# Performance work log

Measured on AMD Instinct MI355X. Metric: run time of the kernel, lower is better.

## Reference

```python
import jax, jax.numpy as jnp
import numpy as np

NUM_BRANCH = 4
KERNEL_SIZES = (1, 3, 5, 7)
NUM_CLASSES = 1000
IN_C = 256
OUT_C = 256


def _cond_conv(x, w, emb, y):
    # x: [B,C,H,W], w: [O,I,k,k], emb: [num_classes,O], y: [B]
    out = jax.lax.conv_general_dilated(
        x, w, window_strides=(1, 1), padding='SAME',
        dimension_numbers=('NCHW', 'OIHW', 'NCHW'))
    return out + emb[y][:, :, None, None]


def setup_inputs() -> dict:
    key = jax.random.key(0)
    ks = jax.random.split(key, 2 + 2 * NUM_BRANCH)
    B, H = 64, 32
    inp = {
        'x': jax.random.normal(ks[0], (B, IN_C, H, H), dtype=jnp.float32),
        'y': jax.random.randint(ks[1], (B,), 0, NUM_CLASSES, dtype=jnp.int64),
        'sample_arc': jax.random.randint(jax.random.fold_in(key, 7), (B,), 0, NUM_BRANCH, dtype=jnp.int64),
    }
    for i, k in enumerate(KERNEL_SIZES):
        fan_in = IN_C * k * k
        inp[f'w{i}'] = jax.random.normal(ks[2 + 2 * i], (OUT_C, IN_C, k, k), dtype=jnp.float32) / np.sqrt(fan_in)
        inp[f'e{i}'] = jax.random.normal(ks[3 + 2 * i], (NUM_CLASSES, OUT_C), dtype=jnp.float32) * 0.02
    return inp


def reference(x, y, sample_arc, w0, w1, w2, w3, e0, e1, e2, e3):
    ws = (w0, w1, w2, w3)
    es = (e0, e1, e2, e3)
    # Compute every branch for every sample (as the original module does),
    # stack along branch dim: [B, num_branch, O, H, W]
    branch_out = jnp.stack([_cond_conv(x, w, e, y) for w, e in zip(ws, es)], axis=1)
    onehot = jax.nn.one_hot(sample_arc, NUM_BRANCH, dtype=x.dtype)  # [B, num_branch]
    # mask-and-sum (one-hot multiply then reduce over branch dim)
    return jnp.einsum('bn,bnchw->bchw', onehot, branch_out)
```

## Files before the change

### kernel.cpp

```cpp
#include <hip/hip_runtime.h>


typedef unsigned short ushort_t;
typedef __attribute__((ext_vector_type(8))) short short8;
typedef __attribute__((ext_vector_type(4))) float f32x4;

#define CIN   256
#define COUT  256
#define HH    32
#define WW    32
#define HW    1024

#define XT_ELEMS   16777216
#define WT_OFF_0   0
#define WT_OFF_1   65536
#define WT_OFF_2   655360
#define WT_OFF_3   2293760
#define WT_ELEMS   5505024
#define TILE_BYTE_OFF ((size_t)(XT_ELEMS + WT_ELEMS) * 2)
#define MAX_TILES  2048
#define WS_NEEDED  (TILE_BYTE_OFF + MAX_TILES * 2 + 64)

#define XS_R_STRIDE 1216
#define XS_C_STRIDE 32
#define XS_ELEMS    12160
#define WR_ELEMS    24576
#define TRASH_ELEMS 2048

__device__ inline ushort_t f2bf(float f) {
    unsigned x = __builtin_bit_cast(unsigned, f);
    unsigned r = (x + 0x7FFFu + ((x >> 16) & 1u)) >> 16;
    return (ushort_t)r;
}

__global__ __launch_bounds__(256) void prep_kernel(
    const float* __restrict__ x,
    const float* __restrict__ w0, const float* __restrict__ w1,
    const float* __restrict__ w2, const float* __restrict__ w3,
    const int* __restrict__ y, const int* __restrict__ arc,
    const float* __restrict__ e0, const float* __restrict__ e1,
    const float* __restrict__ e2, const float* __restrict__ e3,
    float* __restrict__ out,
    ushort_t* __restrict__ xt, ushort_t* __restrict__ wt,
    ushort_t* __restrict__ tiles, unsigned* __restrict__ cnt) {
    __shared__ float lds[2 * 32 * 49];
    const int blk = blockIdx.x;
    const int tid = threadIdx.x;

    if (blk < 4096) {
        const int a   = blk >> 10;
        const int cc  = (blk >> 7) & 7;
        const int oc0 = (blk & 127) * 2;
        const int kk  = (a == 0) ? 1 : (a == 1) ? 9 : (a == 2) ? 25 : 49;
        const float* __restrict__ w = (a == 0) ? w0 : (a == 1) ? w1
                                    : (a == 2) ? w2 : w3;
        const size_t woff = (a == 0) ? WT_OFF_0 : (a == 1) ? WT_OFF_1
                          : (a == 2) ? WT_OFF_2 : WT_OFF_3;
        const int ckk = 32 * kk;
#pragma unroll
        for (int ocq = 0; ocq < 2; ++ocq) {
            const float* src = w + ((size_t)((oc0 + ocq) * CIN + cc * 32)) * kk;
            for (int i = tid; i < ckk; i += 256) lds[ocq * ckk + i] = src[i];
        }
        __syncthreads();
        ushort_t* dst = wt + woff;
        const int F = 2 * kk * 32;
        for (int j = tid; j < F; j += 256) {
            const int ci  = j & 31;
            const int t2  = j >> 5;
            const int khw = t2 % kk;
            const int ocq = t2 / kk;
            dst[((size_t)(cc * kk + khw) * COUT + oc0 + ocq) * 32 + ci] =
                f2bf(lds[ocq * ckk + ci * kk + khw]);
        }
    } else if (blk < 6144) {
        const int id = (blk - 4096) * 256 + tid;
        const int hw = id & 1023;
        const int cc = (id >> 10) & 7;
        const int b  = id >> 13;
        const float* src = x + ((size_t)(b * CIN + cc * 32)) * HW + hw;
        ushort_t* dst = xt + ((size_t)((b * 8 + cc) * HW + hw)) * 32;
#pragma unroll
        for (int v = 0; v < 4; ++v) {
            short8 o;
#pragma unroll
            for (int j = 0; j < 8; ++j)
                o[j] = (short)f2bf(src[(size_t)(v * 8 + j) * HW]);
            *(short8*)(dst + v * 8) = o;
        }
    } else if (blk < 10240) {
        const int z   = blk - 6144;
        const int b   = z >> 6;
        const int a   = arc[b];
        if (a < 2) return;
        const int oc  = (z & 63) * 4 + (tid >> 6);
        const int i   = tid & 63;
        const int cls = y[b];
        const float* __restrict__ e = (a == 2) ? e2 : e3;
        const float ev = e[(size_t)cls * COUT + oc];
        float4 v = make_float4(ev, ev, ev, ev);
        float* ob = out + ((size_t)(b * COUT + oc)) * HW + i * 16;
#pragma unroll
        for (int k = 0; k < 4; ++k) *(float4*)(ob + k * 4) = v;
    } else if (tid < 64) {
        const int lane = tid;
        const int ab = (int)arc[lane];
        unsigned long long m[4];
#pragma unroll
        for (int v = 0; v < 4; ++v) m[v] = __ballot(ab == v);
        int gt = 0;
#pragma unroll
        for (int v = 1; v < 4; ++v) if (v > ab) gt += __popcll(m[v]);
        const unsigned long long eq = (ab == 0) ? m[0] : (ab == 1) ? m[1]
                                    : (ab == 2) ? m[2] : m[3];
        const unsigned long long lower = (lane == 0) ? 0ull
                                       : (~0ull >> (64 - lane));
        const int rank = gt + __popcll(eq & lower);
        const int nh   = __popcll(m[2]) + __popcll(m[3]);
        const bool heavy = (ab >= 2);
        const int myCnt = heavy ? 16 : 8;
        const int start = heavy ? 16 * rank : 16 * nh + 8 * (rank - nh);
        for (int j = 0; j < myCnt; ++j)
            tiles[start + j] = (ushort_t)((lane << 5) | j);
        if (lane == 0) { cnt[0] = 0u; cnt[1] = (unsigned)(512 + 8 * nh); }
    }
}

template <int K, int NCC, bool ATOMIC>
__device__ void conv_body(const ushort_t* __restrict__ xt,
                          const ushort_t* __restrict__ wtb,
                          const float* __restrict__ eb,
                          int b, int cls, int cc0, int r0,
                          float* __restrict__ out,
                          ushort_t* xs, ushort_t* wr, ushort_t* trash) {
    constexpr int KK   = K * K;
    constexpr int PAD  = K / 2;
    constexpr int R    = 4 + 2 * PAD;
    constexpr int ITER = (R * 128) / 256;

    const int tid  = threadIdx.x;
    const int wave = tid >> 6;
    const int lane = tid & 63;
    const int ln   = lane & 15;
    const int q    = lane >> 4;

    f32x4 acc[4][8];
#pragma unroll
    for (int mt = 0; mt < 4; ++mt)
#pragma unroll
        for (int nt = 0; nt < 8; ++nt) acc[mt][nt] = (f32x4)0.0f;

    ushort_t* wrw = wr + wave * (3 * 2048);
    const ushort_t* wsrc = wtb + (size_t)wave * 2048 + (size_t)lane * 8;

    const int t0   = cc0 * KK;
    const int TEND = (cc0 + NCC) * KK;

    auto issue = [&](int idx, ushort_t* dst) {
#pragma unroll
        for (int mt = 0; mt < 4; ++mt)
            __builtin_amdgcn_global_load_lds(
                (const __attribute__((address_space(1))) void*)
                    (wsrc + (size_t)idx * 8192 + mt * 512),
                (__attribute__((address_space(3))) void*)
                    (dst + mt * 512),
                16, 0, 0);
    };

    issue(t0, wrw); issue(t0 + 1, wrw + 2048); issue(t0 + 2, wrw + 4096);

    const ushort_t* xsrc = xt + ((size_t)b * 8) * (HW * 32);

    int rs = 0;
    for (int cc2 = 0; cc2 < NCC; ++cc2) {
        const int cc = cc0 + cc2;
        __syncthreads();
#pragma unroll
        for (int i = 0; i < ITER; ++i) {
            const int id = tid + i * 256;
            const int r  = id >> 7;
            const int gw = (id >> 2) & 31;
            const int g4 = id & 3;
            const int gr = r0 - PAD + r;
            short8 v = (short8)0;
            if (gr >= 0 && gr < HH)
                v = *(const short8*)&xsrc[((size_t)(cc * HW + gr * WW + gw)) * 32 + g4 * 8];
            *(short8*)&xs[r * XS_R_STRIDE + (gw + 3) * XS_C_STRIDE + g4 * 8] = v;
        }
        __syncthreads();

#pragma unroll 1
        for (int kh = 0; kh < K; ++kh) {
#pragma unroll
            for (int kw = 0; kw < K; ++kw) {
                const int t = cc * KK + kh * K + kw;
                asm volatile("s_waitcnt vmcnt(8)" ::: "memory");
                __builtin_amdgcn_sched_barrier(0);
                short8 afc[4];
#pragma unroll
                for (int mt = 0; mt < 4; ++mt)
                    afc[mt] = *(const short8*)&wrw[rs * 2048 + mt * 512 + ln * 32 + q * 8];
                asm volatile("s_waitcnt lgkmcnt(0)" ::: "memory");
                __builtin_amdgcn_sched_barrier(0);
                const bool real = (t + 3 < TEND);
                issue(real ? (t + 3) : t0, real ? (wrw + rs * 2048) : trash);
                short8 bf[8];
#pragma unroll
                for (int nt = 0; nt < 8; ++nt) {
                    const int rl = (nt >> 1) + kh;
                    const int c  = (nt & 1) * 16 + ln + 3 + (kw - PAD);
                    bf[nt] = *(const short8*)&xs[rl * XS_R_STRIDE + c * XS_C_STRIDE + q * 8];
                }
#pragma unroll
                for (int mt = 0; mt < 4; ++mt)
#pragma unroll
                    for (int nt = 0; nt < 8; ++nt)
                        acc[mt][nt] = __builtin_amdgcn_mfma_f32_16x16x32_bf16(
                            afc[mt], bf[nt], acc[mt][nt], 0, 0, 0);
                rs = (rs == 2) ? 0 : rs + 1;
            }
        }
    }

#pragma unroll
    for (int mt = 0; mt < 4; ++mt) {
#pragma unroll
        for (int i = 0; i < 4; ++i) {
            const int oc = wave * 64 + mt * 16 + q * 4 + i;
            float* ob = out + ((size_t)(b * COUT + oc)) * HW;
            if (ATOMIC) {
#pragma unroll
                for (int nt = 0; nt < 8; ++nt) {
                    const int row = r0 + (nt >> 1);
                    const int col = (nt & 1) * 16 + ln;
                    atomicAdd(&ob[row * WW + col], acc[mt][nt][i]);
                }
            } else {
                const float ev = eb[(size_t)cls * COUT + oc];
#pragma unroll
                for (int nt = 0; nt < 8; ++nt) {
                    const int row = r0 + (nt >> 1);
                    const int col = (nt & 1) * 16 + ln;
                    ob[row * WW + col] = acc[mt][nt][i] + ev;
                }
            }
        }
    }
}

__global__ __launch_bounds__(256, 2) void conv_mfma(
    const ushort_t* __restrict__ xt, const ushort_t* __restrict__ wt,
    const int* __restrict__ y, const int* __restrict__ arc,
    const float* __restrict__ e0, const float* __restrict__ e1,
    const float* __restrict__ e2, const float* __restrict__ e3,
    float* __restrict__ out,
    const ushort_t* __restrict__ tiles, unsigned* __restrict__ cnt) {
    __shared__ ushort_t xs[XS_ELEMS];
    __shared__ ushort_t wr[WR_ELEMS];
    __shared__ ushort_t trash[TRASH_ELEMS];
    __shared__ int t_sh;
    const int tid = threadIdx.x;
    const unsigned T = cnt[1];

    for (int i = tid; i < 240; i += 256) {
        const int g    = i & 3;
        const int cell = i >> 2;
        const int cidx = cell % 6;
        const int r    = cell / 6;
        const int col  = (cidx < 3) ? cidx : cidx + 32;
        *(short8*)&xs[r * XS_R_STRIDE + col * XS_C_STRIDE + g * 8] = (short8)0;
    }

    for (;;) {
        if (tid == 0) {
            const unsigned t = atomicAdd(cnt, 1u);
            t_sh = (t < T) ? (int)tiles[t] : -1;
        }
        __syncthreads();
        const int e = t_sh;
        __syncthreads();
        if (e < 0) break;

        const int b   = e >> 5;
        const int j   = e & 31;
        const int a   = __builtin_amdgcn_readfirstlane(arc[b]);
        const int cls = __builtin_amdgcn_readfirstlane(y[b]);
        switch (a) {
            case 0:  conv_body<1, 8, false>(xt, wt + WT_OFF_0, e0, b, cls,
                                            0, (j & 7) << 2, out, xs, wr, trash); break;
            case 1:  conv_body<3, 8, false>(xt, wt + WT_OFF_1, e1, b, cls,
                                            0, (j & 7) << 2, out, xs, wr, trash); break;
            case 2:  conv_body<5, 4, true>(xt, wt + WT_OFF_2, e2, b, cls,
                                           (j & 1) << 2, (j >> 1) << 2, out, xs, wr, trash); break;
            default: conv_body<7, 4, true>(xt, wt + WT_OFF_3, e3, b, cls,
                                           (j & 1) << 2, (j >> 1) << 2, out, xs, wr, trash); break;
        }
    }
}

__global__ __launch_bounds__(256) void cond_conv_direct(
    const float* __restrict__ x, const int* __restrict__ y,
    const int* __restrict__ arc,
    const float* __restrict__ w0, const float* __restrict__ e0,
    const float* __restrict__ w1, const float* __restrict__ e1,
    const float* __restrict__ w2, const float* __restrict__ e2,
    const float* __restrict__ w3, const float* __restrict__ e3,
    float* __restrict__ out) {
    const int b   = blockIdx.x >> 4;
    const int o0  = (blockIdx.x & 15) << 4;
    const int tid = threadIdx.x;
    const int col  = tid & 31;
    const int row0 = tid >> 5;
    int a   = __builtin_amdgcn_readfirstlane(arc[b]);
    int cls = __builtin_amdgcn_readfirstlane(y[b]);
    const int k   = (a == 0) ? 1 : (a == 1) ? 3 : (a == 2) ? 5 : 7;
    const int kk  = k * k;
    const int pad = k >> 1;
    const float* __restrict__ wp = (a == 0) ? w0 : (a == 1) ? w1 : (a == 2) ? w2 : w3;
    const float* __restrict__ ep = (a == 0) ? e0 : (a == 1) ? e1 : (a == 2) ? e2 : e3;
    __shared__ float xsh[8 * HW];
    float acc[16][4];
#pragma unroll
    for (int o = 0; o < 16; ++o)
#pragma unroll
        for (int p = 0; p < 4; ++p) acc[o][p] = 0.f;
    const float* xb = x + (size_t)b * CIN * HW;
    for (int c0 = 0; c0 < CIN; c0 += 8) {
        __syncthreads();
        const float4* src = (const float4*)(xb + c0 * HW);
        float4* dst = (float4*)xsh;
#pragma unroll
        for (int i = 0; i < 8; ++i) dst[tid + (i << 8)] = src[tid + (i << 8)];
        __syncthreads();
        for (int kh = 0; kh < k; ++kh) {
            const int dh = kh - pad;
            int raddr[4]; bool rok[4];
#pragma unroll
            for (int p = 0; p < 4; ++p) {
                const int rr = row0 + 8 * p + dh;
                rok[p] = (rr >= 0) && (rr < HH);
                raddr[p] = (rok[p] ? rr : 0) * WW;
            }
            for (int kw = 0; kw < k; ++kw) {
                const int cc2 = col + kw - pad;
                const bool cok = (cc2 >= 0) && (cc2 < WW);
                const int cofs = cok ? cc2 : 0;
                const int khw = kh * k + kw;
#pragma unroll
                for (int ci = 0; ci < 8; ++ci) {
                    float xv[4];
#pragma unroll
                    for (int p = 0; p < 4; ++p) {
                        const float v = xsh[ci * HW + raddr[p] + cofs];
                        xv[p] = (rok[p] && cok) ? v : 0.f;
                    }
                    const float* wb = wp + (size_t)o0 * CIN * kk + (size_t)(c0 + ci) * kk + khw;
#pragma unroll
                    for (int o = 0; o < 16; ++o) {
                        const float wsv = wb[(size_t)o * CIN * kk];
#pragma unroll
                        for (int p = 0; p < 4; ++p) acc[o][p] += wsv * xv[p];
                    }
                }
            }
        }
    }
    const float* erow = ep + (size_t)cls * COUT + o0;
    float* ob = out + (size_t)(b * COUT + o0) * HW;
#pragma unroll
    for (int o = 0; o < 16; ++o) {
        const float ev = erow[o];
#pragma unroll
        for (int p = 0; p < 4; ++p)
            ob[o * HW + (row0 + 8 * p) * WW + col] = acc[o][p] + ev;
    }
}

extern "C" void kernel_launch(void* const* d_in, const int* in_sizes, int n_in,
                              void* d_out, int out_size, void* d_ws, size_t ws_size,
                              hipStream_t stream) {
    const float* x   = (const float*)d_in[0];
    const int*   y   = (const int*)  d_in[1];
    const int*   arc = (const int*)  d_in[2];
    const float* w0  = (const float*)d_in[3];
    const float* e0  = (const float*)d_in[4];
    const float* w1  = (const float*)d_in[5];
    const float* e1  = (const float*)d_in[6];
    const float* w2  = (const float*)d_in[7];
    const float* e2  = (const float*)d_in[8];
    const float* w3  = (const float*)d_in[9];
    const float* e3  = (const float*)d_in[10];
    float* out = (float*)d_out;
    const int B = in_sizes[1];

    if (ws_size >= WS_NEEDED && B == 64) {
        ushort_t* xt    = (ushort_t*)d_ws;
        ushort_t* wt    = xt + XT_ELEMS;
        ushort_t* tiles = (ushort_t*)((char*)d_ws + TILE_BYTE_OFF);
        unsigned* cnt   = (unsigned*)((char*)d_ws + TILE_BYTE_OFF + MAX_TILES * 2);
        hipLaunchKernelGGL(prep_kernel, dim3(10241), dim3(256), 0, stream,
                           x, w0, w1, w2, w3, y, arc, e0, e1, e2, e3, out,
                           xt, wt, tiles, cnt);
        hipLaunchKernelGGL(conv_mfma, dim3(512), dim3(256), 0, stream,
                           xt, wt, y, arc, e0, e1, e2, e3, out, tiles, cnt);
    } else {
        hipLaunchKernelGGL(cond_conv_direct, dim3(B * 16), dim3(256), 0, stream,
                           x, y, arc, w0, e0, w1, e1, w2, e2, w3, e3, out);
    }
}
```

Before: 372.0 us.

## Reorder conv taps column-major with register-rotated input rows and swizzled weight layout

The inner loop is restructured so the kernel-column shift is outer and kernel-row is inner. Input fragments for four output rows stay in registers and rotate, so each tap loads only two new fragments instead of eight. The weight prep writes a tap-transposed, MFMA-fragment-swizzled layout and the LDS column stride is padded to cut bank conflicts. The weight prefetch ring drops from three stages to two, and the heavy branches split their channels into more tiles (32 per sample) for better load balance, at the cost of more atomic adds and less prefetch slack.

```diff
diff --git a/kernel.cpp b/kernel.cpp
--- a/kernel.cpp
+++ b/kernel.cpp
@@ -21,10 +21,10 @@
 #define MAX_TILES  2048
 #define WS_NEEDED  (TILE_BYTE_OFF + MAX_TILES * 2 + 64)
 
-#define XS_R_STRIDE 1216
-#define XS_C_STRIDE 32
-#define XS_ELEMS    12160
-#define WR_ELEMS    24576
+#define XS_R_STRIDE 1520
+#define XS_C_STRIDE 40
+#define XS_ELEMS    15200
+#define WR_ELEMS    16384
 #define TRASH_ELEMS 2048
 
 __device__ inline ushort_t f2bf(float f) {
@@ -51,7 +51,8 @@
         const int a   = blk >> 10;
         const int cc  = (blk >> 7) & 7;
         const int oc0 = (blk & 127) * 2;
-        const int kk  = (a == 0) ? 1 : (a == 1) ? 9 : (a == 2) ? 25 : 49;
+        const int kf  = (a == 0) ? 1 : (a == 1) ? 3 : (a == 2) ? 5 : 7;
+        const int kk  = kf * kf;
         const float* __restrict__ w = (a == 0) ? w0 : (a == 1) ? w1
                                     : (a == 2) ? w2 : w3;
         const size_t woff = (a == 0) ? WT_OFF_0 : (a == 1) ? WT_OFF_1
@@ -70,7 +71,13 @@
             const int t2  = j >> 5;
             const int khw = t2 % kk;
             const int ocq = t2 / kk;
-            dst[((size_t)(cc * kk + khw) * COUT + oc0 + ocq) * 32 + ci] =
+            const int kh  = khw / kf;
+            const int kw  = khw % kf;
+            const int p   = kw * kf + kh;
+            const int oc  = oc0 + ocq;
+            dst[(size_t)(cc * kk + p) * 8192
+                + (oc >> 6) * 2048 + ((oc >> 4) & 3) * 512
+                + (ci >> 3) * 128 + (oc & 15) * 8 + (ci & 7)] =
                 f2bf(lds[ocq * ckk + ci * kk + khw]);
         }
     } else if (blk < 6144) {
@@ -118,11 +125,11 @@
         const int rank = gt + __popcll(eq & lower);
         const int nh   = __popcll(m[2]) + __popcll(m[3]);
         const bool heavy = (ab >= 2);
-        const int myCnt = heavy ? 16 : 8;
-        const int start = heavy ? 16 * rank : 16 * nh + 8 * (rank - nh);
+        const int myCnt = heavy ? 32 : 8;
+        const int start = heavy ? 32 * rank : 32 * nh + 8 * (rank - nh);
         for (int j = 0; j < myCnt; ++j)
             tiles[start + j] = (ushort_t)((lane << 5) | j);
-        if (lane == 0) { cnt[0] = 0u; cnt[1] = (unsigned)(512 + 8 * nh); }
+        if (lane == 0) { cnt[0] = 0u; cnt[1] = (unsigned)(512 + 24 * nh); }
     }
 }
 
@@ -150,7 +157,7 @@
 #pragma unroll
         for (int nt = 0; nt < 8; ++nt) acc[mt][nt] = (f32x4)0.0f;
 
-    ushort_t* wrw = wr + wave * (3 * 2048);
+    ushort_t* wrw = wr + wave * (2 * 2048);
     const ushort_t* wsrc = wtb + (size_t)wave * 2048 + (size_t)lane * 8;
 
     const int t0   = cc0 * KK;
@@ -167,7 +174,7 @@
                 16, 0, 0);
     };
 
-    issue(t0, wrw); issue(t0 + 1, wrw + 2048); issue(t0 + 2, wrw + 4096);
+    issue(t0, wrw); issue(t0 + 1, wrw + 2048);
 
     const ushort_t* xsrc = xt + ((size_t)b * 8) * (HW * 32);
 
@@ -190,34 +197,49 @@
         __syncthreads();
 
 #pragma unroll 1
-        for (int kh = 0; kh < K; ++kh) {
-#pragma unroll
-            for (int kw = 0; kw < K; ++kw) {
-                const int t = cc * KK + kh * K + kw;
-                asm volatile("s_waitcnt vmcnt(8)" ::: "memory");
+        for (int s = 0; s < K; ++s) {
+            const int cbase = (ln + 3 + s - PAD) * XS_C_STRIDE + q * 8;
+            short8 bw[4][2];
+#pragma unroll
+            for (int r = 0; r < 4; ++r)
+#pragma unroll
+                for (int h = 0; h < 2; ++h)
+                    bw[r][h] = *(const short8*)
+                        &xs[r * XS_R_STRIDE + h * (16 * XS_C_STRIDE) + cbase];
+#pragma unroll
+            for (int kh = 0; kh < K; ++kh) {
+                const int t = cc * KK + s * K + kh;
+                asm volatile("s_waitcnt vmcnt(4)" ::: "memory");
                 __builtin_amdgcn_sched_barrier(0);
                 short8 afc[4];
 #pragma unroll
                 for (int mt = 0; mt < 4; ++mt)
-                    afc[mt] = *(const short8*)&wrw[rs * 2048 + mt * 512 + ln * 32 + q * 8];
+                    afc[mt] = *(const short8*)
+                        &wrw[rs * 2048 + mt * 512 + q * 128 + ln * 8];
                 asm volatile("s_waitcnt lgkmcnt(0)" ::: "memory");
                 __builtin_amdgcn_sched_barrier(0);
-                const bool real = (t + 3 < TEND);
-                issue(real ? (t + 3) : t0, real ? (wrw + rs * 2048) : trash);
-                short8 bf[8];
-#pragma unroll
-                for (int nt = 0; nt < 8; ++nt) {
-                    const int rl = (nt >> 1) + kh;
-                    const int c  = (nt & 1) * 16 + ln + 3 + (kw - PAD);
-                    bf[nt] = *(const short8*)&xs[rl * XS_R_STRIDE + c * XS_C_STRIDE + q * 8];
+                const bool real = (t + 2 < TEND);
+                issue(real ? (t + 2) : t0, real ? (wrw + rs * 2048) : trash);
+                short8 nw[2];
+                if (kh + 1 < K) {
+#pragma unroll
+                    for (int h = 0; h < 2; ++h)
+                        nw[h] = *(const short8*)
+                            &xs[(kh + 4) * XS_R_STRIDE + h * (16 * XS_C_STRIDE) + cbase];
                 }
 #pragma unroll
                 for (int mt = 0; mt < 4; ++mt)
 #pragma unroll
-                    for (int nt = 0; nt < 8; ++nt)
-                        acc[mt][nt] = __builtin_amdgcn_mfma_f32_16x16x32_bf16(
-                            afc[mt], bf[nt], acc[mt][nt], 0, 0, 0);
-                rs = (rs == 2) ? 0 : rs + 1;
+                    for (int m = 0; m < 4; ++m)
+#pragma unroll
+                        for (int h = 0; h < 2; ++h)
+                            acc[mt][m * 2 + h] = __builtin_amdgcn_mfma_f32_16x16x32_bf16(
+                                afc[mt], bw[(kh + m) & 3][h], acc[mt][m * 2 + h], 0, 0, 0);
+                if (kh + 1 < K) {
+                    bw[kh & 3][0] = nw[0];
+                    bw[kh & 3][1] = nw[1];
+                }
+                rs ^= 1;
             }
         }
     }
@@ -290,10 +312,10 @@
                                             0, (j & 7) << 2, out, xs, wr, trash); break;
             case 1:  conv_body<3, 8, false>(xt, wt + WT_OFF_1, e1, b, cls,
                                             0, (j & 7) << 2, out, xs, wr, trash); break;
-            case 2:  conv_body<5, 4, true>(xt, wt + WT_OFF_2, e2, b, cls,
-                                           (j & 1) << 2, (j >> 1) << 2, out, xs, wr, trash); break;
-            default: conv_body<7, 4, true>(xt, wt + WT_OFF_3, e3, b, cls,
-                                           (j & 1) << 2, (j >> 1) << 2, out, xs, wr, trash); break;
+            case 2:  conv_body<5, 2, true>(xt, wt + WT_OFF_2, e2, b, cls,
+                                           (j & 3) << 1, (j >> 2) << 2, out, xs, wr, trash); break;
+            default: conv_body<7, 2, true>(xt, wt + WT_OFF_3, e3, b, cls,
+                                           (j & 3) << 1, (j >> 2) << 2, out, xs, wr, trash); break;
         }
     }
 }
```

Result: no change. 379.1 us (+1.9%).
